# Kernel optimization log

Hardware: AMD Instinct MI355X
Metric: run time of the kernel (lower is better)

The kernel has to match this reference:

```python
import jax, jax.numpy as jnp
import numpy as np


def setup_inputs() -> dict:
    key = jax.random.key(0)
    k1, k2, k3 = jax.random.split(key, 3)
    x = jax.random.normal(k1, (32, 256, 32, 32), dtype=jnp.float32)
    weight = jax.random.normal(k2, (256, 256, 3, 3), dtype=jnp.float32) * 0.05
    bias = jax.random.normal(k3, (256,), dtype=jnp.float32) * 0.01
    return {"x": x, "weight": weight, "bias": bias}


def _forward(x, weight, bias):
    B, cin, n, _ = x.shape
    cout, _, k, _ = weight.shape
    s = (k - 1) // 2
    nf = n // 2 + 1
    bins = n * nf

    # fft shift matrix: exp(-1j*2*pi*s*(i+j)/n), kept rfft columns
    idx = jnp.arange(n)
    shift = idx[None, :] + idx[:, None]                     # (n, n)
    shift_m = jnp.exp(-1j * 2 * jnp.pi * s * shift / n)[:, :nf]
    shift_m = shift_m.reshape(bins, 1, 1).astype(jnp.complex64)

    # xfft: (B, cin, n, nf) -> (bins, cin, B)
    xfft = jnp.fft.rfft2(x)
    xfft = jnp.transpose(xfft, (2, 3, 1, 0)).reshape(bins, cin, B)

    # Hfft: (cout, cin, n, nf) -> (bins, cout, cin), shifted + conj
    Hfft = jnp.fft.rfft2(weight, s=(n, n)).reshape(cout, cin, bins)
    Hfft = shift_m * jnp.conj(jnp.transpose(Hfft, (2, 0, 1)))

    def sq_abs(z):
        return jnp.real(z) ** 2 + jnp.imag(z) ** 2

    RowNorm = jnp.sqrt(jnp.sum(sq_abs(Hfft), axis=2))       # (bins, cout)
    ColNorm = jnp.sqrt(jnp.sum(sq_abs(Hfft), axis=1))       # (bins, cin)

    if cout >= cin:
        RowLoss = jnp.mean((RowNorm - jnp.sqrt(cin / cout)) ** 2)
        ColLoss = jnp.mean((ColNorm - 1.0) ** 2)
        HHT = jnp.einsum('npc,nqc->npq', jnp.conj(Hfft), Hfft)  # (bins, cout, cout)
        mask = jnp.triu(jnp.ones((cout, cout), bool), k=1)
        count = bins * (cout * (cout - 1) // 2)
        AngLoss = jnp.sum(sq_abs(HHT) * mask[None]) / count   # MSE(|HHT[triu]|, 0)
        L = cout * ColLoss + cin * RowLoss + AngLoss
    else:
        RowLoss = jnp.mean((RowNorm - 1.0) ** 2)
        ColLoss = jnp.mean((ColNorm - jnp.sqrt(cout / cin)) ** 2)
        HTH = jnp.einsum('ndp,ndq->npq', jnp.conj(Hfft), Hfft)  # (bins, cin, cin)
        mask = jnp.triu(jnp.ones((cin, cin), bool), k=1)
        count = bins * (cin * (cin - 1) // 2)
        AngLoss = jnp.sum(sq_abs(HTH) * mask[None]) / count
        L = cout * ColLoss + cin * RowLoss + AngLoss

    # per-bin complex matmul: (bins, cout, cin) @ (bins, cin, B) -> (bins, cout, B)
    yfft = Hfft @ xfft
    yfft = jnp.transpose(yfft.reshape(n, nf, cout, B), (3, 2, 0, 1))  # (B, cout, n, nf)
    y = jnp.fft.irfft2(yfft, s=(n, n))
    y = y + bias[None, :, None, None]
    return y, L


def reference(x, weight, bias):
    return _forward(x, weight, bias)
```

## Files before the change

### kernel.cpp

```cpp
#include <hip/hip_runtime.h>
#include <math.h>

typedef __attribute__((ext_vector_type(8)))  short  short8;
typedef __attribute__((ext_vector_type(16))) float  float16;

#define TWO_PI_OVER_32 0.19634954084936207f

static __device__ __forceinline__ unsigned short f2bf(float f) {
    unsigned int u = __float_as_uint(f);
    u = (u + 0x7FFFu + ((u >> 16) & 1u)) >> 16;
    return (unsigned short)u;
}
static __device__ __forceinline__ float bf2f(unsigned short s) {
    return __uint_as_float(((unsigned int)s) << 16);
}

static __device__ __forceinline__ void g2l16(const void* g, void* l) {
    __builtin_amdgcn_global_load_lds(
        (const __attribute__((address_space(1))) unsigned int*)g,
        (__attribute__((address_space(3))) unsigned int*)l, 16, 0, 0);
}

__global__ __launch_bounds__(256) void k_prepx(const float* __restrict__ x,
                                               unsigned short* __restrict__ xb,
                                               const float* __restrict__ w,
                                               unsigned short* __restrict__ wt,
                                               unsigned short* __restrict__ Vb,
                                               float* __restrict__ Drow,
                                               float* __restrict__ Dcol,
                                               float* __restrict__ accum) {
    int tid = threadIdx.x;
    if (blockIdx.x < 4096) {
        int g = blockIdx.x * 256 + tid;
        int c = g & 31, r = (g >> 5) & 31, cig = (g >> 10) & 31, b = g >> 15;
        const float* xp = x + ((b * 256 + cig * 8) * 32 + r) * 32 + c;
        union { unsigned short u[8]; uint4 v; } pk;
        #pragma unroll
        for (int u = 0; u < 8; ++u) pk.u[u] = f2bf(xp[u * 1024]);
        ((uint4*)xb)[g] = pk.v;
        return;
    }
    __shared__ float sdata[45];
    __shared__ float ws2[256 * 9];
    int blk = blockIdx.x - 4096, lane = tid & 63;
    bool colmode = blk >= 256;
    int pc = blk & 255;
    if (blk == 0 && tid < 4) accum[tid] = 0.f;
    if (tid < 45) sdata[tid] = 0.f;

    int p = colmode ? tid : pc;
    int c = colmode ? pc : tid;
    float w9[9];
    #pragma unroll
    for (int t = 0; t < 9; ++t) w9[t] = w[(p * 256 + c) * 9 + t];
    if (!colmode) {
        #pragma unroll
        for (int t = 0; t < 9; ++t) ws2[tid * 9 + t] = w9[t];
    }
    __syncthreads();

    int idx = 0;
    for (int ta = 0; ta < 9; ++ta)
        for (int tb = ta; tb < 9; ++tb) {
            float v = w9[ta] * w9[tb];
            #pragma unroll
            for (int off = 32; off > 0; off >>= 1) v += __shfl_down(v, off);
            if (lane == 0) atomicAdd(&sdata[idx], v);
            ++idx;
        }
    __syncthreads();
    if (tid < 45) (colmode ? Dcol : Drow)[pc * 45 + tid] = sdata[tid];

    if (!colmode) {
        #pragma unroll
        for (int t = 0; t < 9; ++t)
            wt[t * 65536 + (c >> 3) * 2048 + p * 8 + (c & 7)] = f2bf(w9[t]);
        if (tid < 320) {
            int ta = tid >> 5, cig = tid & 31;
            union { unsigned short u[8]; uint4 v; } pk;
            #pragma unroll
            for (int u = 0; u < 8; ++u)
                pk.u[u] = (ta < 9) ? f2bf(ws2[(cig * 8 + u) * 9 + ta]) : (unsigned short)0;
            ((uint4*)Vb)[(p * 10 + ta) * 32 + cig] = pk.v;
        }
    }
}

__global__ __launch_bounds__(256, 2) void k_conv(const unsigned short* __restrict__ xb,
                                                 const unsigned short* __restrict__ wt,
                                                 const float* __restrict__ bias,
                                                 const unsigned short* __restrict__ Vb,
                                                 unsigned short* __restrict__ Gb,
                                                 float* __restrict__ y) {
    __shared__ unsigned short xs[2][640 * 8];
    __shared__ unsigned short wsm[2][1152 * 8];

    const int tid  = threadIdx.x;
    const int lane = tid & 63;
    const int half = lane >> 5;
    const int m    = lane & 31;

    if (blockIdx.x >= 512) {
        int blk = blockIdx.x - 512, I = 0;
        while (blk >= 20 - I) { blk -= 20 - I; ++I; }
        int J = I + blk;
        const int wave = tid >> 6;
        const int wm = wave >> 1, wn = wave & 1;
        const int row0 = I * 128 + wm * 64;
        const int col0 = J * 128 + wn * 64;

        float16 acc[2][2];
        #pragma unroll
        for (int i = 0; i < 2; ++i)
            #pragma unroll
            for (int j = 0; j < 2; ++j)
                #pragma unroll
                for (int r = 0; r < 16; ++r) acc[i][j][r] = 0.f;

        const short8* vb = (const short8*)Vb;
        for (int kc = 0; kc < 16; ++kc) {
            int cig = kc * 2 + half;
            short8 a0 = vb[(row0 + m) * 32 + cig];
            short8 a1 = vb[(row0 + 32 + m) * 32 + cig];
            short8 b0 = vb[(col0 + m) * 32 + cig];
            short8 b1 = vb[(col0 + 32 + m) * 32 + cig];
            acc[0][0] = __builtin_amdgcn_mfma_f32_32x32x16_bf16(a0, b0, acc[0][0], 0, 0, 0);
            acc[0][1] = __builtin_amdgcn_mfma_f32_32x32x16_bf16(a0, b1, acc[0][1], 0, 0, 0);
            acc[1][0] = __builtin_amdgcn_mfma_f32_32x32x16_bf16(a1, b0, acc[1][0], 0, 0, 0);
            acc[1][1] = __builtin_amdgcn_mfma_f32_32x32x16_bf16(a1, b1, acc[1][1], 0, 0, 0);
        }
        #pragma unroll
        for (int i = 0; i < 2; ++i)
            #pragma unroll
            for (int j = 0; j < 2; ++j)
                #pragma unroll
                for (int reg = 0; reg < 16; ++reg) {
                    int crow = (reg & 3) + 8 * (reg >> 2) + 4 * half;
                    Gb[(row0 + i * 32 + crow) * 2560 + col0 + j * 32 + m] =
                        f2bf(acc[i][j][reg]);
                }
        return;
    }

    const int wv   = tid >> 6;
    const int id    = blockIdx.x;
    const int xcd   = id & 7;
    const int local = id >> 3;
    const int b     = xcd * 4 + (local >> 4);
    const int rem   = local & 15;
    const int co0   = (rem & 3) * 64;
    const int r0    = (rem >> 2) * 8;

    float16 acc[2][2];
    #pragma unroll
    for (int i = 0; i < 2; ++i)
        #pragma unroll
        for (int ns = 0; ns < 2; ++ns)
            #pragma unroll
            for (int r = 0; r < 16; ++r) acc[i][ns][r] = 0.f;

    const uint4* xbv = (const uint4*)xb;
    const uint4* wtv = (const uint4*)wt;

    const int cigl = lane >> 5;
    const int coll = lane & 31;

    auto stage = [&](int buf, int kc) {
        uint4* xd = (uint4*)xs[buf];
        uint4* wd = (uint4*)wsm[buf];
        #pragma unroll
        for (int ch = wv; ch < 28; ch += 4) {
            if (ch < 10) {
                int gr = (r0 + ch + 31) & 31;
                g2l16(&xbv[((b * 32 + kc * 2 + cigl) * 32 + gr) * 32 + coll],
                      &xd[ch * 64]);
            } else {
                int wc = ch - 10;
                int t = wc >> 1, cig = wc & 1;
                g2l16(&wtv[t * 8192 + (kc * 2 + cig) * 256 + co0 + lane],
                      &wd[wc * 64]);
            }
        }
    };

    auto compute = [&](int buf) {
        const short8* xsl = (const short8*)xs[buf];
        const short8* wsl = (const short8*)wsm[buf];
        #pragma unroll
        for (int t = 0; t < 9; ++t) {
            const int atv = t / 3, btv = t % 3;
            short8 a0 = wsl[(t * 2 + half) * 64 + m];
            short8 a1 = wsl[(t * 2 + half) * 64 + 32 + m];
            #pragma unroll
            for (int ns = 0; ns < 2; ++ns) {
                int slot = wv * 2 + ns + atv;
                short8 bf = xsl[(slot * 2 + half) * 32 + ((m + btv + 31) & 31)];
                acc[0][ns] = __builtin_amdgcn_mfma_f32_32x32x16_bf16(a0, bf, acc[0][ns], 0, 0, 0);
                acc[1][ns] = __builtin_amdgcn_mfma_f32_32x32x16_bf16(a1, bf, acc[1][ns], 0, 0, 0);
            }
        }
    };

    stage(0, 0);
    #pragma unroll 1
    for (int kc2 = 0; kc2 < 8; ++kc2) {
        __syncthreads();
        stage(1, 2 * kc2 + 1);
        compute(0);
        __syncthreads();
        if (kc2 < 7) stage(0, 2 * kc2 + 2);
        compute(1);
    }

    #pragma unroll
    for (int i = 0; i < 2; ++i) {
        #pragma unroll
        for (int ns = 0; ns < 2; ++ns) {
            int r = r0 + wv * 2 + ns;
            #pragma unroll
            for (int reg = 0; reg < 16; ++reg) {
                int crow = (reg & 3) + 8 * (reg >> 2) + 4 * half;
                int co = co0 + i * 32 + crow;
                y[(b * 256 + co) * 1024 + r * 32 + m] = acc[i][ns][reg] + bias[co];
            }
        }
    }
}

__global__ __launch_bounds__(256) void k_loss(const float* __restrict__ Drow,
                                              const float* __restrict__ Dcol,
                                              const unsigned short* __restrict__ Gb,
                                              float* __restrict__ accum) {
    __shared__ union {
        struct { float coef[45]; float red[2]; } rc;
        struct { unsigned short gs[9 * 2560]; float red; } ang;
    } sh;
    int tid = threadIdx.x;

    if (blockIdx.x < 544) {
        int bin = blockIdx.x;
        int u = bin / 17, v = bin % 17;
        if (tid < 2) sh.rc.red[tid] = 0.f;
        if (tid < 45) {
            int idx = 0, TA = 0, TB = 0;
            for (int ta = 0; ta < 9; ++ta)
                for (int tb = ta; tb < 9; ++tb) {
                    if (idx == tid) { TA = ta; TB = tb; }
                    ++idx;
                }
            int da = TA / 3 - TB / 3;
            int db = TA % 3 - TB % 3;
            float cth = cosf(TWO_PI_OVER_32 * (float)(u * da + v * db));
            sh.rc.coef[tid] = (TA == TB) ? 1.f : 2.f * cth;
        }
        __syncthreads();

        float s1 = 0.f, s2 = 0.f;
        const float* dr = Drow + tid * 45;
        const float* dc = Dcol + tid * 45;
        #pragma unroll
        for (int i = 0; i < 45; ++i) {
            s1 += sh.rc.coef[i] * dr[i];
            s2 += sh.rc.coef[i] * dc[i];
        }
        float e1 = sqrtf(fmaxf(s1, 0.f)) - 1.f; e1 *= e1;
        float e2 = sqrtf(fmaxf(s2, 0.f)) - 1.f; e2 *= e2;
        #pragma unroll
        for (int off = 32; off > 0; off >>= 1) {
            e1 += __shfl_down(e1, off);
            e2 += __shfl_down(e2, off);
        }
        if ((tid & 63) == 0) { atomicAdd(&sh.rc.red[0], e1); atomicAdd(&sh.rc.red[1], e2); }
        __syncthreads();
        if (tid == 0) { atomicAdd(&accum[0], sh.rc.red[0]); atomicAdd(&accum[1], sh.rc.red[1]); }
    } else {
        int p = blockIdx.x - 544;
        if (tid == 0) sh.ang.red = 0.f;
        uint4* gsv = (uint4*)sh.ang.gs;
        const uint4* gbv = (const uint4*)Gb;
        for (int i = tid; i < 2880; i += 256) {
            int rr = i / 320, cc = i - rr * 320;
            gsv[i] = gbv[(p * 10 + rr) * 320 + cc];
        }
        __syncthreads();

        int q = tid;
        float S = 0.f;
        if (q > p) {
            float g5[5][5];
            #pragma unroll
            for (int i = 0; i < 5; ++i)
                #pragma unroll
                for (int j = 0; j < 5; ++j) g5[i][j] = 0.f;
            #pragma unroll
            for (int ta = 0; ta < 9; ++ta)
                #pragma unroll
                for (int tb = 0; tb < 9; ++tb) {
                    float c = bf2f(sh.ang.gs[ta * 2560 + q * 10 + tb]);
                    g5[ta / 3 - tb / 3 + 2][ta % 3 - tb % 3 + 2] += c;
                }
            #pragma unroll
            for (int da = 0; da < 5; ++da) {
                const float* g = g5[da];
                float sq = g[0]*g[0] + g[1]*g[1] + g[2]*g[2] + g[3]*g[3] + g[4]*g[4];
                float cr = g[0]*g[2] + g[1]*g[3] + g[2]*g[4] + g[0]*g[4];
                S += 17.f * sq + 2.f * cr;
            }
            S *= 32.f;
        }
        #pragma unroll
        for (int off = 32; off > 0; off >>= 1) S += __shfl_down(S, off);
        if ((tid & 63) == 0) atomicAdd(&sh.ang.red, S);
        __syncthreads();
        if (tid == 0) atomicAdd(&accum[2], sh.ang.red);
    }
}

__global__ void k_fin(const float* __restrict__ accum, float* __restrict__ out) {
    if (threadIdx.x == 0 && blockIdx.x == 0) {
        float row = accum[0], col = accum[1], ang = accum[2];
        out[8388608] = row / 544.f + col / 544.f + ang / (544.f * 32640.f);
    }
}

extern "C" void kernel_launch(void* const* d_in, const int* in_sizes, int n_in,
                              void* d_out, int out_size, void* d_ws, size_t ws_size,
                              hipStream_t stream) {
    const float* x    = (const float*)d_in[0];
    const float* w    = (const float*)d_in[1];
    const float* bias = (const float*)d_in[2];
    float* out = (float*)d_out;

    char* ws = (char*)d_ws;
    unsigned short* wt = (unsigned short*)ws;
    unsigned short* xb = (unsigned short*)(ws + 1179648);
    unsigned short* Vb = (unsigned short*)(ws + 17956864);
    float* Drow  = (float*)(ws + 19267584);
    float* Dcol  = (float*)(ws + 19313664);
    float* accum = (float*)(ws + 19359744);
    unsigned short* Gb = (unsigned short*)(ws + 19392512);

    k_prepx <<<4608, 256, 0, stream>>>(x, xb, w, wt, Vb, Drow, Dcol, accum);
    k_conv  <<<722, 256, 0, stream>>>(xb, wt, bias, Vb, Gb, out);
    k_loss  <<<800, 256, 0, stream>>>(Drow, Dcol, Gb, accum);
    k_fin   <<<1, 64, 0, stream>>>(accum, out);
}
```

Baseline: 169.8 us.

## Enlarge conv row tile to 16 rows per block and replace atomics with partial sums

Each conv block now covers 16 output rows instead of 8, with 4 row-slots per wave. Every staged input row is reused across up to three kernel-row taps through a reorganised MFMA loop, so weight fetches are amortised over more work and per-block staging overhead drops. The block count is halved and each block uses 72KB of dynamic LDS, which limits occupancy and doubles the accumulator registers per thread. The loss path swaps global atomics for per-bin partial arrays reduced in a wider final kernel, and Drow/Dcol are transposed so the per-thread loads in the loss kernel coalesce.

Measured after the change: 158.8 us. 6.5% less time.

```diff
diff --git a/kernel.cpp b/kernel.cpp
--- a/kernel.cpp
+++ b/kernel.cpp
@@ -27,8 +27,7 @@
                                                unsigned short* __restrict__ wt,
                                                unsigned short* __restrict__ Vb,
                                                float* __restrict__ Drow,
-                                               float* __restrict__ Dcol,
-                                               float* __restrict__ accum) {
+                                               float* __restrict__ Dcol) {
     int tid = threadIdx.x;
     if (blockIdx.x < 4096) {
         int g = blockIdx.x * 256 + tid;
@@ -45,7 +44,6 @@
     int blk = blockIdx.x - 4096, lane = tid & 63;
     bool colmode = blk >= 256;
     int pc = blk & 255;
-    if (blk == 0 && tid < 4) accum[tid] = 0.f;
     if (tid < 45) sdata[tid] = 0.f;
 
     int p = colmode ? tid : pc;
@@ -69,7 +67,7 @@
             ++idx;
         }
     __syncthreads();
-    if (tid < 45) (colmode ? Dcol : Drow)[pc * 45 + tid] = sdata[tid];
+    if (tid < 45) (colmode ? Dcol : Drow)[tid * 256 + pc] = sdata[tid];
 
     if (!colmode) {
         #pragma unroll
@@ -85,6 +83,10 @@
         }
     }
 }
+
+#define XBUF 18432
+#define WBUF 18432
+#define BUFSTRIDE 36864
 
 __global__ __launch_bounds__(256, 2) void k_conv(const unsigned short* __restrict__ xb,
                                                  const unsigned short* __restrict__ wt,
@@ -92,16 +94,15 @@
                                                  const unsigned short* __restrict__ Vb,
                                                  unsigned short* __restrict__ Gb,
                                                  float* __restrict__ y) {
-    __shared__ unsigned short xs[2][640 * 8];
-    __shared__ unsigned short wsm[2][1152 * 8];
+    extern __shared__ unsigned char smem[];
 
     const int tid  = threadIdx.x;
     const int lane = tid & 63;
     const int half = lane >> 5;
     const int m    = lane & 31;
 
-    if (blockIdx.x >= 512) {
-        int blk = blockIdx.x - 512, I = 0;
+    if (blockIdx.x >= 256) {
+        int blk = blockIdx.x - 256, I = 0;
         while (blk >= 20 - I) { blk -= 20 - I; ++I; }
         int J = I + blk;
         const int wave = tid >> 6;
@@ -142,20 +143,20 @@
         return;
     }
 
-    const int wv   = tid >> 6;
+    const int wv    = tid >> 6;
     const int id    = blockIdx.x;
     const int xcd   = id & 7;
     const int local = id >> 3;
-    const int b     = xcd * 4 + (local >> 4);
-    const int rem   = local & 15;
+    const int b     = xcd * 4 + (local >> 3);
+    const int rem   = local & 7;
     const int co0   = (rem & 3) * 64;
-    const int r0    = (rem >> 2) * 8;
-
-    float16 acc[2][2];
+    const int r0    = (rem >> 2) * 16;
+
+    float16 acc[2][4];
     #pragma unroll
     for (int i = 0; i < 2; ++i)
         #pragma unroll
-        for (int ns = 0; ns < 2; ++ns)
+        for (int ns = 0; ns < 4; ++ns)
             #pragma unroll
             for (int r = 0; r < 16; ++r) acc[i][ns][r] = 0.f;
 
@@ -166,16 +167,16 @@
     const int coll = lane & 31;
 
     auto stage = [&](int buf, int kc) {
-        uint4* xd = (uint4*)xs[buf];
-        uint4* wd = (uint4*)wsm[buf];
-        #pragma unroll
-        for (int ch = wv; ch < 28; ch += 4) {
-            if (ch < 10) {
+        uint4* xd = (uint4*)(smem + buf * BUFSTRIDE);
+        uint4* wd = (uint4*)(smem + buf * BUFSTRIDE + XBUF);
+        #pragma unroll
+        for (int ch = wv; ch < 36; ch += 4) {
+            if (ch < 18) {
                 int gr = (r0 + ch + 31) & 31;
                 g2l16(&xbv[((b * 32 + kc * 2 + cigl) * 32 + gr) * 32 + coll],
                       &xd[ch * 64]);
             } else {
-                int wc = ch - 10;
+                int wc = ch - 18;
                 int t = wc >> 1, cig = wc & 1;
                 g2l16(&wtv[t * 8192 + (kc * 2 + cig) * 256 + co0 + lane],
                       &wd[wc * 64]);
@@ -184,19 +185,28 @@
     };
 
     auto compute = [&](int buf) {
-        const short8* xsl = (const short8*)xs[buf];
-        const short8* wsl = (const short8*)wsm[buf];
-        #pragma unroll
-        for (int t = 0; t < 9; ++t) {
-            const int atv = t / 3, btv = t % 3;
-            short8 a0 = wsl[(t * 2 + half) * 64 + m];
-            short8 a1 = wsl[(t * 2 + half) * 64 + 32 + m];
-            #pragma unroll
-            for (int ns = 0; ns < 2; ++ns) {
-                int slot = wv * 2 + ns + atv;
-                short8 bf = xsl[(slot * 2 + half) * 32 + ((m + btv + 31) & 31)];
-                acc[0][ns] = __builtin_amdgcn_mfma_f32_32x32x16_bf16(a0, bf, acc[0][ns], 0, 0, 0);
-                acc[1][ns] = __builtin_amdgcn_mfma_f32_32x32x16_bf16(a1, bf, acc[1][ns], 0, 0, 0);
+        const short8* xsl = (const short8*)(smem + buf * BUFSTRIDE);
+        const short8* wsl = (const short8*)(smem + buf * BUFSTRIDE + XBUF);
+        #pragma unroll
+        for (int btv = 0; btv < 3; ++btv) {
+            short8 a0[3], a1[3];
+            #pragma unroll
+            for (int atv = 0; atv < 3; ++atv) {
+                int t = atv * 3 + btv;
+                a0[atv] = wsl[(t * 2 + half) * 64 + m];
+                a1[atv] = wsl[(t * 2 + half) * 64 + 32 + m];
+            }
+            #pragma unroll
+            for (int s = 0; s < 6; ++s) {
+                short8 bf = xsl[((wv * 4 + s) * 2 + half) * 32 + ((m + btv + 31) & 31)];
+                #pragma unroll
+                for (int atv = 0; atv < 3; ++atv) {
+                    int ns = s - atv;
+                    if (ns >= 0 && ns < 4) {
+                        acc[0][ns] = __builtin_amdgcn_mfma_f32_32x32x16_bf16(a0[atv], bf, acc[0][ns], 0, 0, 0);
+                        acc[1][ns] = __builtin_amdgcn_mfma_f32_32x32x16_bf16(a1[atv], bf, acc[1][ns], 0, 0, 0);
+                    }
+                }
             }
         }
     };
@@ -215,8 +225,8 @@
     #pragma unroll
     for (int i = 0; i < 2; ++i) {
         #pragma unroll
-        for (int ns = 0; ns < 2; ++ns) {
-            int r = r0 + wv * 2 + ns;
+        for (int ns = 0; ns < 4; ++ns) {
+            int r = r0 + wv * 4 + ns;
             #pragma unroll
             for (int reg = 0; reg < 16; ++reg) {
                 int crow = (reg & 3) + 8 * (reg >> 2) + 4 * half;
@@ -230,7 +240,9 @@
 __global__ __launch_bounds__(256) void k_loss(const float* __restrict__ Drow,
                                               const float* __restrict__ Dcol,
                                               const unsigned short* __restrict__ Gb,
-                                              float* __restrict__ accum) {
+                                              float* __restrict__ rowp,
+                                              float* __restrict__ colp,
+                                              float* __restrict__ angp) {
     __shared__ union {
         struct { float coef[45]; float red[2]; } rc;
         struct { unsigned short gs[9 * 2560]; float red; } ang;
@@ -256,12 +268,12 @@
         __syncthreads();
 
         float s1 = 0.f, s2 = 0.f;
-        const float* dr = Drow + tid * 45;
-        const float* dc = Dcol + tid * 45;
+        const float* dr = Drow + tid;
+        const float* dc = Dcol + tid;
         #pragma unroll
         for (int i = 0; i < 45; ++i) {
-            s1 += sh.rc.coef[i] * dr[i];
-            s2 += sh.rc.coef[i] * dc[i];
+            s1 += sh.rc.coef[i] * dr[i * 256];
+            s2 += sh.rc.coef[i] * dc[i * 256];
         }
         float e1 = sqrtf(fmaxf(s1, 0.f)) - 1.f; e1 *= e1;
         float e2 = sqrtf(fmaxf(s2, 0.f)) - 1.f; e2 *= e2;
@@ -272,7 +284,7 @@
         }
         if ((tid & 63) == 0) { atomicAdd(&sh.rc.red[0], e1); atomicAdd(&sh.rc.red[1], e2); }
         __syncthreads();
-        if (tid == 0) { atomicAdd(&accum[0], sh.rc.red[0]); atomicAdd(&accum[1], sh.rc.red[1]); }
+        if (tid == 0) { rowp[bin] = sh.rc.red[0]; colp[bin] = sh.rc.red[1]; }
     } else {
         int p = blockIdx.x - 544;
         if (tid == 0) sh.ang.red = 0.f;
@@ -312,14 +324,35 @@
         for (int off = 32; off > 0; off >>= 1) S += __shfl_down(S, off);
         if ((tid & 63) == 0) atomicAdd(&sh.ang.red, S);
         __syncthreads();
-        if (tid == 0) atomicAdd(&accum[2], sh.ang.red);
-    }
-}
-
-__global__ void k_fin(const float* __restrict__ accum, float* __restrict__ out) {
-    if (threadIdx.x == 0 && blockIdx.x == 0) {
-        float row = accum[0], col = accum[1], ang = accum[2];
-        out[8388608] = row / 544.f + col / 544.f + ang / (544.f * 32640.f);
+        if (tid == 0) angp[p] = sh.ang.red;
+    }
+}
+
+__global__ __launch_bounds__(256) void k_fin(const float* __restrict__ rowp,
+                                             const float* __restrict__ colp,
+                                             const float* __restrict__ angp,
+                                             float* __restrict__ out) {
+    __shared__ float sred[3][4];
+    int tid = threadIdx.x;
+    float r = 0.f, c = 0.f, a = 0.f;
+    for (int i = tid; i < 544; i += 256) { r += rowp[i]; c += colp[i]; }
+    a = angp[tid];
+    #pragma unroll
+    for (int off = 32; off > 0; off >>= 1) {
+        r += __shfl_down(r, off);
+        c += __shfl_down(c, off);
+        a += __shfl_down(a, off);
+    }
+    if ((tid & 63) == 0) {
+        int wv = tid >> 6;
+        sred[0][wv] = r; sred[1][wv] = c; sred[2][wv] = a;
+    }
+    __syncthreads();
+    if (tid == 0) {
+        float R = sred[0][0] + sred[0][1] + sred[0][2] + sred[0][3];
+        float C = sred[1][0] + sred[1][1] + sred[1][2] + sred[1][3];
+        float A = sred[2][0] + sred[2][1] + sred[2][2] + sred[2][3];
+        out[8388608] = R / 544.f + C / 544.f + A / (544.f * 32640.f);
     }
 }
 
@@ -337,11 +370,20 @@
     unsigned short* Vb = (unsigned short*)(ws + 17956864);
     float* Drow  = (float*)(ws + 19267584);
     float* Dcol  = (float*)(ws + 19313664);
-    float* accum = (float*)(ws + 19359744);
+    float* rowp  = (float*)(ws + 19359744);
+    float* colp  = (float*)(ws + 19361920);
+    float* angp  = (float*)(ws + 19364096);
     unsigned short* Gb = (unsigned short*)(ws + 19392512);
 
-    k_prepx <<<4608, 256, 0, stream>>>(x, xb, w, wt, Vb, Drow, Dcol, accum);
-    k_conv  <<<722, 256, 0, stream>>>(xb, wt, bias, Vb, Gb, out);
-    k_loss  <<<800, 256, 0, stream>>>(Drow, Dcol, Gb, accum);
-    k_fin   <<<1, 64, 0, stream>>>(accum, out);
-}
+    static bool smem_cfg = false;
+    if (!smem_cfg) {
+        hipFuncSetAttribute(reinterpret_cast<const void*>(k_conv),
+                            hipFuncAttributeMaxDynamicSharedMemorySize, 73728);
+        smem_cfg = true;
+    }
+
+    k_prepx <<<4608, 256, 0, stream>>>(x, xb, w, wt, Vb, Drow, Dcol);
+    k_conv  <<<466, 256, 73728, stream>>>(xb, wt, bias, Vb, Gb, out);
+    k_loss  <<<800, 256, 0, stream>>>(Drow, Dcol, Gb, rowp, colp, angp);
+    k_fin   <<<1, 256, 0, stream>>>(rowp, colp, angp, out);
+}
```
